# Kernel tuning notes

Hardware: AMD Instinct MI355X
Metric: run time of the kernel (lower is better)

Reference implementation:

```python
import jax, jax.numpy as jnp
import numpy as np

D_MODEL = 1024
N_HEADS = 16
D_K = D_MODEL // N_HEADS  # 64
SCALE = 0.125             # attention_scale = 1/sqrt(d_k)
ROPE_BASE = 10000.0
NEG_INF = -1e30


def setup_inputs() -> dict:
    key = jax.random.key(0)
    k1, k2, k3 = jax.random.split(key, 3)
    B, S = 2, 2048
    x = jax.random.normal(k1, (B, S, D_MODEL), jnp.float32)
    # torch Linear(d_model, 3*d_model, bias=False): stored here as [in, out]
    w_qkv = jax.random.normal(k2, (D_MODEL, 3 * D_MODEL), jnp.float32) * (D_MODEL ** -0.5)
    w_o = jax.random.normal(k3, (D_MODEL, D_MODEL), jnp.float32) * (D_MODEL ** -0.5)
    return {"x": x, "w_qkv": w_qkv, "w_o": w_o}


def _rotary(x):
    # x: [B, H, S, D]; standard half-split rotary over sequence positions
    S, D = x.shape[2], x.shape[3]
    inv_freq = 1.0 / (ROPE_BASE ** (jnp.arange(0, D, 2, dtype=jnp.float32) / D))  # [D/2]
    freqs = jnp.arange(S, dtype=jnp.float32)[:, None] * inv_freq[None, :]          # [S, D/2]
    cos = jnp.cos(freqs)[None, None]  # [1,1,S,D/2]
    sin = jnp.sin(freqs)[None, None]
    x1, x2 = jnp.split(x, 2, axis=-1)
    return jnp.concatenate([x1 * cos + x2 * sin, -x1 * sin + x2 * cos], axis=-1).astype(x.dtype)


def reference(x, w_qkv, w_o):
    B, S, _ = x.shape
    qkv = x @ w_qkv                                        # [B,S,3*D_MODEL]
    qkv = qkv.reshape(B, S, 3, N_HEADS, D_K).transpose(2, 0, 3, 1, 4)  # [3,B,H,S,Dk]
    q, k, v = qkv[0], qkv[1], qkv[2]
    q = _rotary(q)
    k = _rotary(k)
    scores = jnp.einsum('bhqd,bhkd->bhqk', q, k) * SCALE   # [B,H,S,S]
    causal = jnp.tril(jnp.ones((S, S), dtype=bool))
    scores = jnp.where(causal, scores, NEG_INF)
    attn = jax.nn.softmax(scores, axis=-1)
    out = jnp.einsum('bhqk,bhkd->bhqd', attn, v)           # [B,H,S,Dk]
    out = out.transpose(0, 2, 1, 3).reshape(B, S, D_MODEL)
    return out @ w_o
```

## Files before the change

kernel.cpp:

```cpp
#include <hip/hip_runtime.h>

typedef short bf16x8 __attribute__((ext_vector_type(8)));
typedef short bf16x4 __attribute__((ext_vector_type(4)));
typedef float f32x4 __attribute__((ext_vector_type(4)));
typedef float f32x16 __attribute__((ext_vector_type(16)));
typedef int i32x4 __attribute__((ext_vector_type(4)));

#define DEVI static __device__ __forceinline__

DEVI unsigned short f2b(float f) {
  unsigned u = __float_as_uint(f);
  u += 0x7FFFu + ((u >> 16) & 1u);
  return (unsigned short)(u >> 16);
}

DEVI void gload16(const void* g, void* l) {
  __builtin_amdgcn_global_load_lds((const __attribute__((address_space(1))) void*)g,
                                   (__attribute__((address_space(3))) void*)l, 16, 0, 0);
}

DEVI void pl32swap(int a, int b, int& outa, int& outb) {
#if __has_builtin(__builtin_amdgcn_permlane32_swap)
  auto r = __builtin_amdgcn_permlane32_swap(a, b, false, false);
  outa = ((const int*)&r)[0];
  outb = ((const int*)&r)[1];
#else
  int bp = __shfl_xor(b, 32);
  int ap = __shfl_xor(a, 32);
  outa = (threadIdx.x & 32) ? bp : a;
  outb = (threadIdx.x & 32) ? b : ap;
#endif
}

DEVI float halfmax(float x) {
  int o0, o1;
  pl32swap(__float_as_int(x), __float_as_int(x), o0, o1);
  return fmaxf(__int_as_float(o0), __int_as_float(o1));
}
DEVI float halfsum(float x) {
  int o0, o1;
  pl32swap(__float_as_int(x), __float_as_int(x), o0, o1);
  return __int_as_float(o0) + __int_as_float(o1);
}

__global__ void rope_table_kernel(float* __restrict__ ct, float* __restrict__ st) {
  int i = blockIdx.x * 256 + threadIdx.x;
  int s = i >> 5, j = i & 31;
  float inv = powf(10000.0f, -(float)j * (1.0f / 32.0f));
  float a = (float)s * inv;
  ct[i] = cosf(a);
  st[i] = sinf(a);
}

__global__ void cvt_x_kernel(const float* __restrict__ x, unsigned short* __restrict__ xb) {
  int i = blockIdx.x * 256 + threadIdx.x;
  float4 v = ((const float4*)x)[i];
  ushort4 o;
  o.x = f2b(v.x); o.y = f2b(v.y); o.z = f2b(v.z); o.w = f2b(v.w);
  ((ushort4*)xb)[i] = o;
}

__global__ void transpose_kernel(const float* __restrict__ W, unsigned short* __restrict__ WT,
                                 int K, int N) {
  __shared__ float tile[32][33];
  int n0 = blockIdx.x * 32, k0 = blockIdx.y * 32;
  int tx = threadIdx.x, ty = threadIdx.y;
#pragma unroll
  for (int i = 0; i < 32; i += 8)
    tile[ty + i][tx] = W[(size_t)(k0 + ty + i) * N + n0 + tx];
  __syncthreads();
#pragma unroll
  for (int i = 0; i < 32; i += 8)
    WT[(size_t)(n0 + ty + i) * K + k0 + tx] = f2b(tile[tx][ty + i]);
}

DEVI void gemm_mainloop(const unsigned short* __restrict__ A, const unsigned short* __restrict__ B,
                        unsigned short* As, unsigned short* Bs,
                        int m0, int n0, int lane, int wid, int wr, int wc,
                        f32x4 acc[4][4]) {
  const int srow = lane >> 3;
  const int scc = ((lane & 7) ^ srow) * 8;
  auto stage = [&](int k0, int nb) {
    unsigned short* Ad = As + nb * 8192;
    unsigned short* Bd = Bs + nb * 8192;
#pragma unroll
    for (int i = 0; i < 4; ++i) {
      const int c = i * 4 + wid;
      const int row = c * 8 + srow;
      gload16(A + (size_t)(m0 + row) * 1024 + k0 + scc, (char*)Ad + c * 1024);
      gload16(B + (size_t)(n0 + row) * 1024 + k0 + scc, (char*)Bd + c * 1024);
    }
  };
  stage(0, 0);
  __syncthreads();
  const int rx = lane & 7;
  for (int t = 0; t < 16; ++t) {
    const int cur = t & 1;
    if (t < 15) stage((t + 1) * 64, cur ^ 1);
    const unsigned short* Ab = As + cur * 8192;
    const unsigned short* Bb = Bs + cur * 8192;
#pragma unroll
    for (int kk = 0; kk < 64; kk += 32) {
      const int cc = (((kk >> 3) + (lane >> 4)) ^ rx) * 8;
      bf16x8 a[4], b[4];
#pragma unroll
      for (int mi = 0; mi < 4; ++mi)
        a[mi] = *(const bf16x8*)&Ab[(wr * 64 + mi * 16 + (lane & 15)) * 64 + cc];
#pragma unroll
      for (int ni = 0; ni < 4; ++ni)
        b[ni] = *(const bf16x8*)&Bb[(wc * 64 + ni * 16 + (lane & 15)) * 64 + cc];
#pragma unroll
      for (int mi = 0; mi < 4; ++mi)
#pragma unroll
        for (int ni = 0; ni < 4; ++ni)
          acc[mi][ni] = __builtin_amdgcn_mfma_f32_16x16x32_bf16(a[mi], b[ni], acc[mi][ni], 0, 0, 0);
    }
    __syncthreads();
  }
}

__global__ __launch_bounds__(256) void gemm_qkv_kernel(
    const unsigned short* __restrict__ Xb, const unsigned short* __restrict__ WT,
    const float* __restrict__ ct, const float* __restrict__ st,
    unsigned short* __restrict__ Qb, unsigned short* __restrict__ Kb,
    unsigned short* __restrict__ VTb) {
  __shared__ unsigned short As[2][128 * 64];
  __shared__ unsigned short Bs[2][128 * 64];
  const int lane = threadIdx.x & 63, wid = threadIdx.x >> 6;
  const int m0 = blockIdx.y * 128, n0 = blockIdx.x * 128;
  const int wr = wid >> 1, wc = wid & 1;
  f32x4 acc[4][4] = {};
  gemm_mainloop(Xb, WT, &As[0][0], &Bs[0][0], m0, n0, lane, wid, wr, wc, acc);

  const int n_base = n0 + wc * 64;
  const int t = n_base >> 10;
  const int h = (n_base & 1023) >> 6;
  if (t < 2) {
    unsigned short* dst = (t == 0) ? Qb : Kb;
#pragma unroll
    for (int mi = 0; mi < 4; ++mi) {
      const int mrow = m0 + wr * 64 + mi * 16 + ((lane >> 4) << 2);
#pragma unroll
      for (int r = 0; r < 4; ++r) {
        const int m = mrow + r;
        const int s = m & 2047, bb = m >> 11;
        const size_t base = ((size_t)(bb * 16 + h) * 2048 + s) * 64;
#pragma unroll
        for (int ni = 0; ni < 2; ++ni) {
          const int j = ni * 16 + (lane & 15);
          const float c = ct[s * 32 + j], sn = st[s * 32 + j];
          const float x1 = acc[mi][ni][r], x2 = acc[mi][ni + 2][r];
          dst[base + j]      = f2b(x1 * c + x2 * sn);
          dst[base + j + 32] = f2b(-x1 * sn + x2 * c);
        }
      }
    }
  } else {
#pragma unroll
    for (int mi = 0; mi < 4; ++mi) {
      const int mrow = m0 + wr * 64 + mi * 16 + ((lane >> 4) << 2);
      const int s = mrow & 2047, bb = mrow >> 11;
#pragma unroll
      for (int ni = 0; ni < 4; ++ni) {
        const int d = ni * 16 + (lane & 15);
        ushort4 o;
        o.x = f2b(acc[mi][ni][0]); o.y = f2b(acc[mi][ni][1]);
        o.z = f2b(acc[mi][ni][2]); o.w = f2b(acc[mi][ni][3]);
        *(ushort4*)&VTb[((size_t)(bb * 16 + h) * 64 + d) * 2048 + s] = o;
      }
    }
  }
}

DEVI void stage128(const unsigned short* __restrict__ Kh, const unsigned short* __restrict__ Vh,
                   int kbase, unsigned char* buf , int tid) {
  const int r = tid >> 3, c = tid & 7, cc = c ^ (r & 7);
  const int dst = (tid & ~63) * 16;
#pragma unroll
  for (int q = 0; q < 2; ++q) {
    unsigned char* b = buf + q * 16384;
    gload16(Kh + (size_t)(kbase + q * 64 + r) * 64 + cc * 8, b + dst);
    gload16(Vh + (size_t)r * 2048 + kbase + q * 64 + cc * 8, b + 8192 + dst);
  }
}

DEVI void attn_sub(const unsigned char* __restrict__ bufK, const unsigned char* __restrict__ bufV,
                   const bf16x8 qf[4], int s32, int kglob, bool diag, int qg, int ln, int hi,
                   float& m2, float& l_run, f32x16& acc0, f32x16& acc1) {
  const float C = 0.125f * 1.44269504f;
  const int rx = ln & 7;
  bf16x8 kf[4];
#pragma unroll
  for (int j = 0; j < 4; ++j) {
    const int cc = (2 * j + hi) ^ rx;
    kf[j] = *(const bf16x8*)(bufK + (s32 * 32 + ln) * 128 + cc * 16);
  }
  bf16x8 v0[2], v1[2];
#pragma unroll
  for (int p = 0; p < 2; ++p) {
    const int cc = (4 * s32 + 2 * p + hi) ^ rx;
    v0[p] = *(const bf16x8*)(bufV + ln * 128 + cc * 16);
    v1[p] = *(const bf16x8*)(bufV + (ln + 32) * 128 + cc * 16);
  }

  f32x16 stv = {};
  __builtin_amdgcn_s_setprio(1);
  stv = __builtin_amdgcn_mfma_f32_32x32x16_bf16(kf[0], qf[0], stv, 0, 0, 0);
  stv = __builtin_amdgcn_mfma_f32_32x32x16_bf16(kf[1], qf[1], stv, 0, 0, 0);
  stv = __builtin_amdgcn_mfma_f32_32x32x16_bf16(kf[2], qf[2], stv, 0, 0, 0);
  stv = __builtin_amdgcn_mfma_f32_32x32x16_bf16(kf[3], qf[3], stv, 0, 0, 0);
  __builtin_amdgcn_s_setprio(0);

  float sraw[16];
#pragma unroll
  for (int r = 0; r < 16; ++r) sraw[r] = stv[r];
  if (diag) {
#pragma unroll
    for (int r = 0; r < 16; ++r) {
      const int kg = kglob + (r & 3) + ((r >> 2) << 3) + (hi << 2);
      if (kg > qg) sraw[r] = -1e30f;
    }
  }
  float mraw = sraw[0];
#pragma unroll
  for (int r = 1; r < 16; ++r) mraw = fmaxf(mraw, sraw[r]);
  const float mloc = halfmax(mraw * C);
  if (__any(mloc > m2 + 11.5416f)) {
    const float mnew = fmaxf(m2, mloc);
    const float sc = exp2f(m2 - mnew);
    l_run *= sc;
#pragma unroll
    for (int r = 0; r < 16; ++r) { acc0[r] *= sc; acc1[r] *= sc; }
    m2 = mnew;
  }
  float p[16], ps = 0.f;
#pragma unroll
  for (int r = 0; r < 16; ++r) { p[r] = exp2f(fmaf(sraw[r], C, -m2)); ps += p[r]; }
  l_run += halfsum(ps);

  int cw[8];
#pragma unroll
  for (int i = 0; i < 8; ++i)
    asm("v_cvt_pk_bf16_f32 %0, %1, %2" : "=v"(cw[i]) : "v"(p[2 * i]), "v"(p[2 * i + 1]));
  int a0, a1, b0, b1, a2, a3, b2, b3;
  pl32swap(cw[0], cw[2], a0, b0);
  pl32swap(cw[1], cw[3], a1, b1);
  pl32swap(cw[4], cw[6], a2, b2);
  pl32swap(cw[5], cw[7], a3, b3);
  const bf16x8 pa0 = __builtin_bit_cast(bf16x8, (i32x4){a0, a1, b0, b1});
  const bf16x8 pa1 = __builtin_bit_cast(bf16x8, (i32x4){a2, a3, b2, b3});

  __builtin_amdgcn_s_setprio(1);
  acc0 = __builtin_amdgcn_mfma_f32_32x32x16_bf16(v0[0], pa0, acc0, 0, 0, 0);
  acc0 = __builtin_amdgcn_mfma_f32_32x32x16_bf16(v0[1], pa1, acc0, 0, 0, 0);
  acc1 = __builtin_amdgcn_mfma_f32_32x32x16_bf16(v1[0], pa0, acc1, 0, 0, 0);
  acc1 = __builtin_amdgcn_mfma_f32_32x32x16_bf16(v1[1], pa1, acc1, 0, 0, 0);
  __builtin_amdgcn_s_setprio(0);
}

DEVI void write_partial(float* M, int slot, const f32x16& a0, const f32x16& a1,
                        float m2, float l) {
#pragma unroll
  for (int r = 0; r < 16; ++r) { M[slot + r] = a0[r]; M[slot + 16 + r] = a1[r]; }
  M[slot + 32] = m2;
  M[slot + 33] = l;
}

DEVI void write_merged(unsigned short* __restrict__ Ob, const float* M, int slot,
                       const f32x16& acc0, const f32x16& acc1, float m2, float l_run,
                       int bh, int q0, int ln, int hi) {
  const float mp = M[slot + 32], lp = M[slot + 33];
  const float m = fmaxf(m2, mp);
  const float eo = exp2f(m2 - m), ep = exp2f(mp - m);
  const float il = 1.0f / (l_run * eo + lp * ep);
  const int b = bh >> 4, h = bh & 15;
  unsigned short* ob = Ob + ((size_t)(b * 2048 + q0 + ln)) * 1024 + h * 64;
#pragma unroll
  for (int g = 0; g < 4; ++g) {
    ushort4 o0, o1;
    o0.x = f2b((acc0[4 * g + 0] * eo + M[slot + 4 * g + 0] * ep) * il);
    o0.y = f2b((acc0[4 * g + 1] * eo + M[slot + 4 * g + 1] * ep) * il);
    o0.z = f2b((acc0[4 * g + 2] * eo + M[slot + 4 * g + 2] * ep) * il);
    o0.w = f2b((acc0[4 * g + 3] * eo + M[slot + 4 * g + 3] * ep) * il);
    o1.x = f2b((acc1[4 * g + 0] * eo + M[slot + 16 + 4 * g + 0] * ep) * il);
    o1.y = f2b((acc1[4 * g + 1] * eo + M[slot + 16 + 4 * g + 1] * ep) * il);
    o1.z = f2b((acc1[4 * g + 2] * eo + M[slot + 16 + 4 * g + 2] * ep) * il);
    o1.w = f2b((acc1[4 * g + 3] * eo + M[slot + 16 + 4 * g + 3] * ep) * il);
    *(ushort4*)&ob[8 * g + 4 * hi]      = o0;
    *(ushort4*)&ob[32 + 8 * g + 4 * hi] = o1;
  }
}

__global__ __launch_bounds__(512) void attn_kernel(
    const unsigned short* __restrict__ Qb, const unsigned short* __restrict__ Kb,
    const unsigned short* __restrict__ VTb, unsigned short* __restrict__ Ob) {
  __shared__ unsigned char smem[2][2][16384];
  const int tid = threadIdx.x;
  const int lane = tid & 63, wid = tid >> 6;
  const int ln = lane & 31, hi = lane >> 5;
  const int s = wid & 3, half = wid >> 2;
  const int bh = blockIdx.x;
  const int p = blockIdx.y;
  const int jA = 15 - p, jB = p;
  const unsigned short* Qh = Qb + (size_t)bh * 2048 * 64;
  const unsigned short* Kh = Kb + (size_t)bh * 2048 * 64;
  const unsigned short* Vh = VTb + (size_t)bh * 64 * 2048;

  f32x16 aA0 = {}, aA1 = {}, aB0 = {}, aB1 = {};
  float mA = -1e30f, lA = 0.f, mB = -1e30f, lB = 0.f;
  int it = 0;

  auto load_q = [&](int q0, bf16x8 qf[4]) {
    const unsigned short* pq = Qh + (size_t)(q0 + ln) * 64 + hi * 8;
#pragma unroll
    for (int t = 0; t < 4; ++t) qf[t] = *(const bf16x8*)(pq + t * 16);
  };
  auto run_phase = [&](int j, const bf16x8 qf[4], f32x16& acc0, f32x16& acc1,
                       float& m2, float& l_run, int q0, int nextFirst) {
    const int qg = q0 + ln;
    const int top = q0 >> 5;
    for (int kb = 0; kb <= j; ++kb, ++it) {
      const int nxt = (kb < j) ? (kb + 1) * 128 : nextFirst;
      if (nxt >= 0) stage128(Kh, Vh, nxt, &smem[(it + 1) & 1][0][0], tid);
      const unsigned char* bufK = &smem[it & 1][half][0];
      const unsigned char* bufV = bufK + 8192;
      const int t64 = 2 * kb + half;
#pragma unroll
      for (int s32 = 0; s32 < 2; ++s32) {
        const int g32 = 2 * t64 + s32;
        if (g32 <= top)
          attn_sub(bufK, bufV, qf, s32, g32 * 32, g32 == top, qg, ln, hi, m2, l_run, acc0, acc1);
      }
      __syncthreads();
    }
  };

  bf16x8 qfA[4];
  load_q(jA * 128 + s * 32, qfA);
  stage128(Kh, Vh, 0, &smem[0][0][0], tid);
  __syncthreads();
  run_phase(jA, qfA, aA0, aA1, mA, lA, jA * 128 + s * 32, 0);
  bf16x8 qfB[4];
  load_q(jB * 128 + s * 32, qfB);
  run_phase(jB, qfB, aB0, aB1, mB, lB, jB * 128 + s * 32, -1);

  float* M = (float*)&smem[0][0][0];
  const int slot = (s * 64 + lane) * 34;
  if (half == 1) write_partial(M, slot, aA0, aA1, mA, lA);
  __syncthreads();
  if (half == 0) write_merged(Ob, M, slot, aA0, aA1, mA, lA, bh, jA * 128 + s * 32, ln, hi);
  __syncthreads();
  if (half == 0) write_partial(M, slot, aB0, aB1, mB, lB);
  __syncthreads();
  if (half == 1) write_merged(Ob, M, slot, aB0, aB1, mB, lB, bh, jB * 128 + s * 32, ln, hi);
}

__global__ __launch_bounds__(256) void gemm_out_kernel(
    const unsigned short* __restrict__ Ob, const unsigned short* __restrict__ WoT,
    float* __restrict__ out) {
  __shared__ unsigned short As[2][128 * 64];
  __shared__ unsigned short Bs[2][128 * 64];
  const int lane = threadIdx.x & 63, wid = threadIdx.x >> 6;
  const int m0 = blockIdx.y * 128, n0 = blockIdx.x * 128;
  const int wr = wid >> 1, wc = wid & 1;
  f32x4 acc[4][4] = {};
  gemm_mainloop(Ob, WoT, &As[0][0], &Bs[0][0], m0, n0, lane, wid, wr, wc, acc);
#pragma unroll
  for (int mi = 0; mi < 4; ++mi) {
    const int mrow = m0 + wr * 64 + mi * 16 + ((lane >> 4) << 2);
#pragma unroll
    for (int ni = 0; ni < 4; ++ni) {
      const int n = n0 + wc * 64 + ni * 16 + (lane & 15);
#pragma unroll
      for (int r = 0; r < 4; ++r)
        out[(size_t)(mrow + r) * 1024 + n] = acc[mi][ni][r];
    }
  }
}

extern "C" void kernel_launch(void* const* d_in, const int* in_sizes, int n_in,
                              void* d_out, int out_size, void* d_ws, size_t ws_size,
                              hipStream_t stream) {
  const float* x     = (const float*)d_in[0];
  const float* w_qkv = (const float*)d_in[1];
  const float* w_o   = (const float*)d_in[2];
  float* out = (float*)d_out;
  char* ws = (char*)d_ws;

  const size_t MB = 1 << 20;
  float* ct = (float*)(ws);
  float* st = (float*)(ws + (256 << 10));
  unsigned short* Xb  = (unsigned short*)(ws + (512 << 10));
  unsigned short* WqT = (unsigned short*)(ws + (512 << 10) + 8  * MB);
  unsigned short* WoT = (unsigned short*)(ws + (512 << 10) + 14 * MB);
  unsigned short* Qb  = (unsigned short*)(ws + (512 << 10) + 16 * MB);
  unsigned short* Kb  = (unsigned short*)(ws + (512 << 10) + 24 * MB);
  unsigned short* VTb = (unsigned short*)(ws + (512 << 10) + 32 * MB);
  unsigned short* Ob  = Xb;

  rope_table_kernel<<<dim3(256), dim3(256), 0, stream>>>(ct, st);
  cvt_x_kernel<<<dim3(4096), dim3(256), 0, stream>>>(x, Xb);
  transpose_kernel<<<dim3(96, 32), dim3(32, 8), 0, stream>>>(w_qkv, WqT, 1024, 3072);
  transpose_kernel<<<dim3(32, 32), dim3(32, 8), 0, stream>>>(w_o, WoT, 1024, 1024);
  gemm_qkv_kernel<<<dim3(24, 32), dim3(256), 0, stream>>>(Xb, WqT, ct, st, Qb, Kb, VTb);
  attn_kernel<<<dim3(32, 8), dim3(512), 0, stream>>>(Qb, Kb, VTb, Ob);
  gemm_out_kernel<<<dim3(8, 32), dim3(256), 0, stream>>>(Ob, WoT, out);
}
```

Measured before the change: 130.9 us.

## Enlarge QKV GEMM tile to 256x256 and restructure prefetch pipeline

```diff
diff --git a/kernel.cpp b/kernel.cpp
--- a/kernel.cpp
+++ b/kernel.cpp
@@ -74,72 +74,78 @@
     WT[(size_t)(n0 + ty + i) * K + k0 + tx] = f2b(tile[tx][ty + i]);
 }
 
-DEVI void gemm_mainloop(const unsigned short* __restrict__ A, const unsigned short* __restrict__ B,
-                        unsigned short* As, unsigned short* Bs,
-                        int m0, int n0, int lane, int wid, int wr, int wc,
-                        f32x4 acc[4][4]) {
-  const int srow = lane >> 3;
-  const int scc = ((lane & 7) ^ srow) * 8;
-  auto stage = [&](int k0, int nb) {
-    unsigned short* Ad = As + nb * 8192;
-    unsigned short* Bd = Bs + nb * 8192;
-#pragma unroll
-    for (int i = 0; i < 4; ++i) {
-      const int c = i * 4 + wid;
-      const int row = c * 8 + srow;
-      gload16(A + (size_t)(m0 + row) * 1024 + k0 + scc, (char*)Ad + c * 1024);
-      gload16(B + (size_t)(n0 + row) * 1024 + k0 + scc, (char*)Bd + c * 1024);
-    }
-  };
-  stage(0, 0);
-  __syncthreads();
-  const int rx = lane & 7;
-  for (int t = 0; t < 16; ++t) {
-    const int cur = t & 1;
-    if (t < 15) stage((t + 1) * 64, cur ^ 1);
-    const unsigned short* Ab = As + cur * 8192;
-    const unsigned short* Bb = Bs + cur * 8192;
-#pragma unroll
-    for (int kk = 0; kk < 64; kk += 32) {
-      const int cc = (((kk >> 3) + (lane >> 4)) ^ rx) * 8;
-      bf16x8 a[4], b[4];
-#pragma unroll
-      for (int mi = 0; mi < 4; ++mi)
-        a[mi] = *(const bf16x8*)&Ab[(wr * 64 + mi * 16 + (lane & 15)) * 64 + cc];
-#pragma unroll
-      for (int ni = 0; ni < 4; ++ni)
-        b[ni] = *(const bf16x8*)&Bb[(wc * 64 + ni * 16 + (lane & 15)) * 64 + cc];
-#pragma unroll
-      for (int mi = 0; mi < 4; ++mi)
-#pragma unroll
-        for (int ni = 0; ni < 4; ++ni)
-          acc[mi][ni] = __builtin_amdgcn_mfma_f32_16x16x32_bf16(a[mi], b[ni], acc[mi][ni], 0, 0, 0);
-    }
-    __syncthreads();
-  }
-}
-
-__global__ __launch_bounds__(256) void gemm_qkv_kernel(
+__global__ __launch_bounds__(512, 2) void gemm_qkv_kernel(
     const unsigned short* __restrict__ Xb, const unsigned short* __restrict__ WT,
     const float* __restrict__ ct, const float* __restrict__ st,
     unsigned short* __restrict__ Qb, unsigned short* __restrict__ Kb,
     unsigned short* __restrict__ VTb) {
-  __shared__ unsigned short As[2][128 * 64];
-  __shared__ unsigned short Bs[2][128 * 64];
-  const int lane = threadIdx.x & 63, wid = threadIdx.x >> 6;
-  const int m0 = blockIdx.y * 128, n0 = blockIdx.x * 128;
-  const int wr = wid >> 1, wc = wid & 1;
-  f32x4 acc[4][4] = {};
-  gemm_mainloop(Xb, WT, &As[0][0], &Bs[0][0], m0, n0, lane, wid, wr, wc, acc);
+  __shared__ unsigned short As[2][256 * 64];
+  __shared__ unsigned short Bs[2][256 * 64];
+  const int tid = threadIdx.x;
+  const int lane = tid & 63, wid = tid >> 6;
+  const int m0 = blockIdx.y * 256, n0 = blockIdx.x * 256;
+  const int wr = wid >> 2, wc = wid & 3;
+  const int srow = lane >> 3;
+  const int scc = ((lane & 7) ^ srow) * 8;
+  const int rx = lane & 7;
+
+  f32x4 acc[8][4] = {};
+
+  auto stage = [&](int k0, int nb) {
+    unsigned short* Ad = As[nb];
+    unsigned short* Bd = Bs[nb];
+#pragma unroll
+    for (int i = 0; i < 4; ++i) {
+      const int c = i * 8 + wid;
+      const int row = c * 8 + srow;
+      gload16(Xb + (size_t)(m0 + row) * 1024 + k0 + scc, (char*)Ad + c * 1024);
+      gload16(WT + (size_t)(n0 + row) * 1024 + k0 + scc, (char*)Bd + c * 1024);
+    }
+  };
+  auto compute = [&](int nb) {
+    const unsigned short* Ab = As[nb];
+    const unsigned short* Bb = Bs[nb];
+#pragma unroll
+    for (int kk = 0; kk < 64; kk += 32) {
+      const int cc = (((kk >> 3) + (lane >> 4)) ^ rx) * 8;
+      bf16x8 a[8], b[4];
+#pragma unroll
+      for (int mi = 0; mi < 8; ++mi)
+        a[mi] = *(const bf16x8*)&Ab[(wr * 128 + mi * 16 + (lane & 15)) * 64 + cc];
+#pragma unroll
+      for (int ni = 0; ni < 4; ++ni)
+        b[ni] = *(const bf16x8*)&Bb[(wc * 64 + ni * 16 + (lane & 15)) * 64 + cc];
+      __builtin_amdgcn_s_setprio(1);
+#pragma unroll
+      for (int mi = 0; mi < 8; ++mi)
+#pragma unroll
+        for (int ni = 0; ni < 4; ++ni)
+          acc[mi][ni] = __builtin_amdgcn_mfma_f32_16x16x32_bf16(a[mi], b[ni], acc[mi][ni], 0, 0, 0);
+      __builtin_amdgcn_s_setprio(0);
+    }
+  };
+
+  stage(0, 0);
+  stage(64, 1);
+  for (int t = 0; t < 15; ++t) {
+    asm volatile("s_waitcnt vmcnt(8)" ::: "memory");
+    __builtin_amdgcn_s_barrier();
+    compute(t & 1);
+    __builtin_amdgcn_s_barrier();
+    if (t < 14) stage((t + 2) * 64, t & 1);
+  }
+  asm volatile("s_waitcnt vmcnt(0)" ::: "memory");
+  __builtin_amdgcn_s_barrier();
+  compute(1);
 
   const int n_base = n0 + wc * 64;
-  const int t = n_base >> 10;
+  const int ty = n_base >> 10;
   const int h = (n_base & 1023) >> 6;
-  if (t < 2) {
-    unsigned short* dst = (t == 0) ? Qb : Kb;
-#pragma unroll
-    for (int mi = 0; mi < 4; ++mi) {
-      const int mrow = m0 + wr * 64 + mi * 16 + ((lane >> 4) << 2);
+  if (ty < 2) {
+    unsigned short* dst = (ty == 0) ? Qb : Kb;
+#pragma unroll
+    for (int mi = 0; mi < 8; ++mi) {
+      const int mrow = m0 + wr * 128 + mi * 16 + ((lane >> 4) << 2);
 #pragma unroll
       for (int r = 0; r < 4; ++r) {
         const int m = mrow + r;
@@ -157,8 +163,8 @@
     }
   } else {
 #pragma unroll
-    for (int mi = 0; mi < 4; ++mi) {
-      const int mrow = m0 + wr * 64 + mi * 16 + ((lane >> 4) << 2);
+    for (int mi = 0; mi < 8; ++mi) {
+      const int mrow = m0 + wr * 128 + mi * 16 + ((lane >> 4) << 2);
       const int s = mrow & 2047, bb = mrow >> 11;
 #pragma unroll
       for (int ni = 0; ni < 4; ++ni) {
@@ -170,6 +176,60 @@
       }
     }
   }
+}
+
+DEVI void gemm_mainloop(const unsigned short* __restrict__ A, const unsigned short* __restrict__ B,
+                        unsigned short* As, unsigned short* Bs,
+                        int m0, int n0, int lane, int wid, int wr, int wc,
+                        f32x4 acc[4][4]) {
+  const int srow = lane >> 3;
+  const int scc = ((lane & 7) ^ srow) * 8;
+  const int rx = lane & 7;
+  auto stage = [&](int k0, int nb) {
+    unsigned short* Ad = As + nb * 8192;
+    unsigned short* Bd = Bs + nb * 8192;
+#pragma unroll
+    for (int i = 0; i < 4; ++i) {
+      const int c = i * 4 + wid;
+      const int row = c * 8 + srow;
+      gload16(A + (size_t)(m0 + row) * 1024 + k0 + scc, (char*)Ad + c * 1024);
+      gload16(B + (size_t)(n0 + row) * 1024 + k0 + scc, (char*)Bd + c * 1024);
+    }
+  };
+  auto compute = [&](int nb) {
+    const unsigned short* Ab = As + nb * 8192;
+    const unsigned short* Bb = Bs + nb * 8192;
+#pragma unroll
+    for (int kk = 0; kk < 64; kk += 32) {
+      const int cc = (((kk >> 3) + (lane >> 4)) ^ rx) * 8;
+      bf16x8 a[4], b[4];
+#pragma unroll
+      for (int mi = 0; mi < 4; ++mi)
+        a[mi] = *(const bf16x8*)&Ab[(wr * 64 + mi * 16 + (lane & 15)) * 64 + cc];
+#pragma unroll
+      for (int ni = 0; ni < 4; ++ni)
+        b[ni] = *(const bf16x8*)&Bb[(wc * 64 + ni * 16 + (lane & 15)) * 64 + cc];
+      __builtin_amdgcn_s_setprio(1);
+#pragma unroll
+      for (int mi = 0; mi < 4; ++mi)
+#pragma unroll
+        for (int ni = 0; ni < 4; ++ni)
+          acc[mi][ni] = __builtin_amdgcn_mfma_f32_16x16x32_bf16(a[mi], b[ni], acc[mi][ni], 0, 0, 0);
+      __builtin_amdgcn_s_setprio(0);
+    }
+  };
+  stage(0, 0);
+  stage(64, 1);
+  for (int t = 0; t < 15; ++t) {
+    asm volatile("s_waitcnt vmcnt(8)" ::: "memory");
+    __builtin_amdgcn_s_barrier();
+    compute(t & 1);
+    __builtin_amdgcn_s_barrier();
+    if (t < 14) stage((t + 2) * 64, t & 1);
+  }
+  asm volatile("s_waitcnt vmcnt(0)" ::: "memory");
+  __builtin_amdgcn_s_barrier();
+  compute(1);
 }
 
 DEVI void stage128(const unsigned short* __restrict__ Kh, const unsigned short* __restrict__ Vh,
@@ -402,7 +462,7 @@
   cvt_x_kernel<<<dim3(4096), dim3(256), 0, stream>>>(x, Xb);
   transpose_kernel<<<dim3(96, 32), dim3(32, 8), 0, stream>>>(w_qkv, WqT, 1024, 3072);
   transpose_kernel<<<dim3(32, 32), dim3(32, 8), 0, stream>>>(w_o, WoT, 1024, 1024);
-  gemm_qkv_kernel<<<dim3(24, 32), dim3(256), 0, stream>>>(Xb, WqT, ct, st, Qb, Kb, VTb);
+  gemm_qkv_kernel<<<dim3(12, 16), dim3(512), 0, stream>>>(Xb, WqT, ct, st, Qb, Kb, VTb);
   attn_kernel<<<dim3(32, 8), dim3(512), 0, stream>>>(Qb, Kb, VTb, Ob);
   gemm_out_kernel<<<dim3(8, 32), dim3(256), 0, stream>>>(Ob, WoT, out);
 }
```

Measured after the change: 123.5 us. 1.06x faster.
